# Optimization experiments

Hardware: AMD Instinct MI355X
Metric: run time of the kernel (lower is better)

The kernel has to match this reference:

```python
import jax, jax.numpy as jnp
import numpy as np

B, N, NIN, NHID, D = 8, 2048, 256, 256, 64  # head = 1 (required by squeeze())


def setup_inputs() -> dict:
    key = jax.random.key(0)
    ks = jax.random.split(key, 12)
    xn = lambda k, shape, s=1.0: jax.random.normal(k, shape, jnp.float32) * s
    xav = lambda fi, fo: (2.0 / (fi + fo)) ** 0.5  # xavier_normal std
    return {
        "inputs": xn(ks[0], (B, N, NIN)),
        "fc1_w": xn(ks[1], (NHID, NIN), xav(NIN, NHID)),
        "fc1_b": jnp.full((NHID,), 0.1, jnp.float32),
        "fc2_w": xn(ks[2], (NHID, NHID), xav(NHID, NHID)),
        "fc2_b": jnp.full((NHID,), 0.1, jnp.float32),
        "bn_g": 1.0 + 0.1 * xn(ks[3], (NHID,)),
        "bn_b": 0.1 * xn(ks[4], (NHID,)),
        "bn_mean": 0.1 * xn(ks[5], (NHID,)),
        "bn_var": jax.random.uniform(ks[6], (NHID,), jnp.float32, 0.5, 1.5),
        "wq_w": xn(ks[7], (D, NHID), xav(NHID, D)),
        "wq_b": jnp.full((D,), 0.1, jnp.float32),
        "wk_w": xn(ks[8], (D, NHID), xav(NHID, D)),
        "wk_b": jnp.full((D,), 0.1, jnp.float32),
        "mlp2_w": xn(ks[9], (1, 2 * D), xav(2 * D, 1)),
        "mlp2_b": jnp.full((1,), 0.1, jnp.float32),
    }


def reference(inputs, fc1_w, fc1_b, fc2_w, fc2_b, bn_g, bn_b, bn_mean, bn_var,
              wq_w, wq_b, wk_w, wk_b, mlp2_w, mlp2_b):
    # MLP: Linear -> ELU -> (dropout off, eval) -> Linear -> ELU -> BatchNorm1d (eval, running stats)
    x = jax.nn.elu(jnp.einsum('bni,hi->bnh', inputs, fc1_w) + fc1_b)
    x = jax.nn.elu(jnp.einsum('bnh,oh->bno', x, fc2_w) + fc2_b)
    X = (x - bn_mean) * jax.lax.rsqrt(bn_var + 1e-5) * bn_g + bn_b  # [B,N,NHID]
    # Q/K projections (head=1 -> shapes [B,N,D])
    Xq = jnp.einsum('bnh,dh->bnd', X, wq_w) + wq_b
    Xk = jnp.einsum('bnh,dh->bnd', X, wk_w) + wk_b
    # Original: cat([NK, NQ], -1) over all (i,j) pairs then Linear(2D -> 1).
    # Algebraically identical decomposition: probs[b,i,j] = Xk[b,j].wk_half + Xq[b,i].wq_half + bias
    wk_half, wq_half = mlp2_w[0, :D], mlp2_w[0, D:]
    sk = Xk @ wk_half  # [B,N]  (varies with j, the K/column index)
    sq = Xq @ wq_half  # [B,N]  (varies with i, the Q/row index)
    probs = sq[:, :, None] + sk[:, None, :] + mlp2_b[0]  # [B,N,N]
    return probs
```

## Files before the change

### kernel.cpp

```cpp
#include <hip/hip_runtime.h>
#include <hip/hip_bf16.h>
#include <math.h>

typedef __bf16 bf16x8 __attribute__((ext_vector_type(8)));
typedef float  f32x4  __attribute__((ext_vector_type(4)));
typedef unsigned int u32;
typedef u32 u32x4 __attribute__((ext_vector_type(4)));
typedef unsigned short u16;

#define WS_STG1  0
#define WS_STG2  32768
#define WS_UQ    65536
#define WS_UK    65792
#define WS_CONST 66048
#define WS_SQ    66064
#define WS_SK    82448

__device__ __forceinline__ float elu1(float x) {
    return x > 0.f ? x : (__expf(x) - 1.f);
}

__global__ void prep_all(const float* __restrict__ w1, const float* __restrict__ w2,
                         const float* __restrict__ bn_g, const float* __restrict__ bn_b,
                         const float* __restrict__ bn_mean, const float* __restrict__ bn_var,
                         const float* __restrict__ wq_w, const float* __restrict__ wq_b,
                         const float* __restrict__ wk_w, const float* __restrict__ wk_b,
                         const float* __restrict__ mlp2_w, const float* __restrict__ mlp2_b,
                         float* __restrict__ ws) {
    if (blockIdx.x == 0) {
        __shared__ float redq[256], redk[256];
        const int h = threadIdx.x;
        float s  = bn_g[h] * rsqrtf(bn_var[h] + 1e-5f);
        float tt = bn_b[h] - bn_mean[h] * s;
        float vq = 0.f, vk = 0.f;
        #pragma unroll
        for (int d = 0; d < 64; ++d) {
            vq += wq_w[d * 256 + h] * mlp2_w[64 + d];
            vk += wk_w[d * 256 + h] * mlp2_w[d];
        }
        ws[WS_UQ + h] = s * vq;
        ws[WS_UK + h] = s * vk;
        redq[h] = tt * vq;
        redk[h] = tt * vk;
        __syncthreads();
        for (int st = 128; st > 0; st >>= 1) {
            if (h < st) { redq[h] += redq[h + st]; redk[h] += redk[h + st]; }
            __syncthreads();
        }
        if (h == 0) {
            float cq = 0.f, ck = 0.f;
            for (int d = 0; d < 64; ++d) {
                cq += wq_b[d] * mlp2_w[64 + d];
                ck += wk_b[d] * mlp2_w[d];
            }
            ws[WS_CONST + 0] = redq[0] + cq;
            ws[WS_CONST + 1] = redk[0] + ck;
            ws[WS_CONST + 2] = mlp2_b[0];
        }
        return;
    }
    const int bid = blockIdx.x - 1;
    const int m   = bid >> 3;
    const int kt  = bid & 7;
    const float* src = m ? w2 : w1;
    __bf16* stg = (__bf16*)(ws + (m ? WS_STG2 : WS_STG1));
    const int tid = threadIdx.x;
    #pragma unroll
    for (int it = 0; it < 4; ++it) {
        int idx = it * 256 + tid;
        int nt = idx >> 6, l = idx & 63;
        int lr = l & 15, lk = l >> 4;
        const float* sp = src + (nt * 16 + lr) * 256 + kt * 32 + lk * 8;
        bf16x8 hi;
        #pragma unroll
        for (int j = 0; j < 8; ++j) hi[j] = (__bf16)sp[j];
        *(bf16x8*)(stg + (kt * 16 + nt) * 512 + l * 8) = hi;
    }
}

__global__ __launch_bounds__(512, 4) void main_mfma(const float* __restrict__ inp,
                                                    const float* __restrict__ b1,
                                                    const float* __restrict__ b2,
                                                    float* __restrict__ ws) {
    __shared__ u32 X1p[8192];
    __shared__ float redq[128], redk[128];

    const int tid = threadIdx.x;
    const int l   = tid & 63;
    const int gw  = tid >> 6;
    const int w   = gw & 3;
    const int p   = gw >> 2;
    const int lr  = l & 15;
    const int lk  = l >> 4;
    const int rows0 = blockIdx.x * 32;
    const int koff  = blockIdx.x & 7;
    const int n0  = w * 64;

    const __bf16* s1 = (const __bf16*)(ws + WS_STG1);
    const __bf16* s2 = (const __bf16*)(ws + WS_STG2);
    const float*  arow = inp + (size_t)(rows0 + p * 16 + lr) * 256 + lk * 8;

    f32x4 acc[4];

    #pragma unroll
    for (int nt = 0; nt < 4; ++nt) acc[nt] = (f32x4)0.f;

    bf16x8 bc[4];
    float4 f0, f1;
    {
        const int kts = koff;
        #pragma unroll
        for (int nt = 0; nt < 4; ++nt)
            bc[nt] = *(const bf16x8*)(s1 + ((kts * 16 + w * 4 + nt) << 9) + l * 8);
        f0 = ((const float4*)(arow + kts * 32))[0];
        f1 = ((const float4*)(arow + kts * 32))[1];
    }

    #pragma unroll
    for (int kt = 0; kt < 8; ++kt) {
        bf16x8 bn[4];
        float4 g0 = f0, g1 = f1;
        if (kt < 7) {
            const int ktn = (kt + 1 + koff) & 7;
            #pragma unroll
            for (int nt = 0; nt < 4; ++nt)
                bn[nt] = *(const bf16x8*)(s1 + ((ktn * 16 + w * 4 + nt) << 9) + l * 8);
            g0 = ((const float4*)(arow + ktn * 32))[0];
            g1 = ((const float4*)(arow + ktn * 32))[1];
        } else {
            #pragma unroll
            for (int nt = 0; nt < 4; ++nt) bn[nt] = bc[nt];
        }
        bf16x8 ah, al;
        {
            float fv[8] = {f0.x,f0.y,f0.z,f0.w,f1.x,f1.y,f1.z,f1.w};
            #pragma unroll
            for (int j = 0; j < 8; ++j) {
                __bf16 hv = (__bf16)fv[j];
                ah[j] = hv;
                al[j] = (__bf16)(fv[j] - (float)hv);
            }
        }
        #pragma unroll
        for (int nt = 0; nt < 4; ++nt) {
            acc[nt] = __builtin_amdgcn_mfma_f32_16x16x32_bf16(ah, bc[nt], acc[nt], 0, 0, 0);
            acc[nt] = __builtin_amdgcn_mfma_f32_16x16x32_bf16(al, bc[nt], acc[nt], 0, 0, 0);
        }
        #pragma unroll
        for (int nt = 0; nt < 4; ++nt) bc[nt] = bn[nt];
        f0 = g0; f1 = g1;
    }
    #pragma unroll
    for (int nt = 0; nt < 4; ++nt) {
        int col = n0 + nt * 16 + lr;
        float bb = b1[col];
        #pragma unroll
        for (int r = 0; r < 4; ++r) {
            int row = p * 16 + lk * 4 + r;
            float v = elu1(acc[nt][r] + bb);
            __bf16 hv = (__bf16)v;
            __bf16 lv = (__bf16)(v - (float)hv);
            u32 pk = ((u32)__builtin_bit_cast(u16, hv) << 16) | __builtin_bit_cast(u16, lv);
            int ob = row * 1024 + ((col * 4) ^ ((row & 15) << 4));
            *(u32*)((char*)X1p + ob) = pk;
        }
    }
    __syncthreads();

    #pragma unroll
    for (int nt = 0; nt < 4; ++nt) acc[nt] = (f32x4)0.f;

    const int base = (p * 16 + lr) * 1024;
    const int sw   = lr << 4;

    bf16x8 bc2[4];
    #pragma unroll
    for (int nt = 0; nt < 4; ++nt)
        bc2[nt] = *(const bf16x8*)(s2 + ((koff * 16 + w * 4 + nt) << 9) + l * 8);

    #pragma unroll
    for (int kt = 0; kt < 8; ++kt) {
        const int kts = (kt + koff) & 7;
        bf16x8 bn[4];
        if (kt < 7) {
            const int ktn = (kt + 1 + koff) & 7;
            #pragma unroll
            for (int nt = 0; nt < 4; ++nt)
                bn[nt] = *(const bf16x8*)(s2 + ((ktn * 16 + w * 4 + nt) << 9) + l * 8);
        } else {
            #pragma unroll
            for (int nt = 0; nt < 4; ++nt) bn[nt] = bc2[nt];
        }
        int cb = kts * 128 + lk * 32;
        u32x4 q0 = *(const u32x4*)((const char*)X1p + base + (cb ^ sw));
        u32x4 q1 = *(const u32x4*)((const char*)X1p + base + ((cb + 16) ^ sw));
        u32 hw0 = __builtin_amdgcn_perm(q0.y, q0.x, 0x07060302u);
        u32 hw1 = __builtin_amdgcn_perm(q0.w, q0.z, 0x07060302u);
        u32 hw2 = __builtin_amdgcn_perm(q1.y, q1.x, 0x07060302u);
        u32 hw3 = __builtin_amdgcn_perm(q1.w, q1.z, 0x07060302u);
        u32 lw0 = __builtin_amdgcn_perm(q0.y, q0.x, 0x05040100u);
        u32 lw1 = __builtin_amdgcn_perm(q0.w, q0.z, 0x05040100u);
        u32 lw2 = __builtin_amdgcn_perm(q1.y, q1.x, 0x05040100u);
        u32 lw3 = __builtin_amdgcn_perm(q1.w, q1.z, 0x05040100u);
        u32x4 hh = {hw0, hw1, hw2, hw3};
        u32x4 ll = {lw0, lw1, lw2, lw3};
        bf16x8 ah = __builtin_bit_cast(bf16x8, hh);
        bf16x8 al = __builtin_bit_cast(bf16x8, ll);
        #pragma unroll
        for (int nt = 0; nt < 4; ++nt) {
            acc[nt] = __builtin_amdgcn_mfma_f32_16x16x32_bf16(ah, bc2[nt], acc[nt], 0, 0, 0);
            acc[nt] = __builtin_amdgcn_mfma_f32_16x16x32_bf16(al, bc2[nt], acc[nt], 0, 0, 0);
        }
        #pragma unroll
        for (int nt = 0; nt < 4; ++nt) bc2[nt] = bn[nt];
    }

    float sqp[4] = {0.f,0.f,0.f,0.f};
    float skp[4] = {0.f,0.f,0.f,0.f};
    const float* uq = ws + WS_UQ;
    const float* uk = ws + WS_UK;
    #pragma unroll
    for (int nt = 0; nt < 4; ++nt) {
        int col = n0 + nt * 16 + lr;
        float bb = b2[col], qc = uq[col], kc = uk[col];
        #pragma unroll
        for (int r = 0; r < 4; ++r) {
            float v = elu1(acc[nt][r] + bb);
            sqp[r] += v * qc;
            skp[r] += v * kc;
        }
    }
    #pragma unroll
    for (int mm = 8; mm >= 1; mm >>= 1) {
        #pragma unroll
        for (int r = 0; r < 4; ++r) {
            sqp[r] += __shfl_xor(sqp[r], mm);
            skp[r] += __shfl_xor(skp[r], mm);
        }
    }
    if (lr == 0) {
        #pragma unroll
        for (int r = 0; r < 4; ++r) {
            int rl = lk * 4 + r;
            redq[gw * 16 + rl] = sqp[r];
            redk[gw * 16 + rl] = skp[r];
        }
    }
    __syncthreads();
    if (tid < 32) {
        int pp = tid >> 4, rl = tid & 15;
        float s = ws[WS_CONST + 0];
        #pragma unroll
        for (int ww = 0; ww < 4; ++ww) s += redq[(pp * 4 + ww) * 16 + rl];
        ws[WS_SQ + rows0 + tid] = s;
    } else if (tid < 64) {
        int rr = tid - 32;
        int pp = rr >> 4, rl = rr & 15;
        float s = ws[WS_CONST + 1];
        #pragma unroll
        for (int ww = 0; ww < 4; ++ww) s += redk[(pp * 4 + ww) * 16 + rl];
        ws[WS_SK + rows0 + rr] = s;
    }
}

__global__ __launch_bounds__(256) void broadcast_out(const float* __restrict__ ws,
                                                     float* __restrict__ out) {
    __shared__ float skL[2048];
    const int bi = blockIdx.x;
    const int b = bi >> 8;
    const int chunk = bi & 255;
    const int tid = threadIdx.x;

    float4* skL4 = (float4*)skL;
    const float4* skb4 = (const float4*)(ws + WS_SK + b * 2048);
    #pragma unroll
    for (int it = 0; it < 2; ++it) skL4[it * 256 + tid] = skb4[it * 256 + tid];
    __syncthreads();

    const float mb = ws[WS_CONST + 2];
    const int i0 = chunk * 8;
    #pragma unroll
    for (int i = 0; i < 8; ++i) {
        float sval = ws[WS_SQ + b * 2048 + i0 + i] + mb;
        float4* orow = (float4*)(out + ((size_t)(b * 2048 + i0 + i)) * 2048);
        #pragma unroll
        for (int hh = 0; hh < 2; ++hh) {
            int j4 = hh * 256 + tid;
            float4 v = skL4[j4];
            orow[j4] = make_float4(sval + v.x, sval + v.y, sval + v.z, sval + v.w);
        }
    }
}

extern "C" void kernel_launch(void* const* d_in, const int* in_sizes, int n_in,
                              void* d_out, int out_size, void* d_ws, size_t ws_size,
                              hipStream_t stream) {
    const float* inputs  = (const float*)d_in[0];
    const float* fc1_w   = (const float*)d_in[1];
    const float* fc1_b   = (const float*)d_in[2];
    const float* fc2_w   = (const float*)d_in[3];
    const float* fc2_b   = (const float*)d_in[4];
    const float* bn_g    = (const float*)d_in[5];
    const float* bn_b    = (const float*)d_in[6];
    const float* bn_mean = (const float*)d_in[7];
    const float* bn_var  = (const float*)d_in[8];
    const float* wq_w    = (const float*)d_in[9];
    const float* wq_b    = (const float*)d_in[10];
    const float* wk_w    = (const float*)d_in[11];
    const float* wk_b    = (const float*)d_in[12];
    const float* mlp2_w  = (const float*)d_in[13];
    const float* mlp2_b  = (const float*)d_in[14];
    float* ws  = (float*)d_ws;
    float* out = (float*)d_out;

    hipLaunchKernelGGL(prep_all, dim3(17), dim3(256), 0, stream,
                       fc1_w, fc2_w, bn_g, bn_b, bn_mean, bn_var,
                       wq_w, wq_b, wk_w, wk_b, mlp2_w, mlp2_b, ws);
    hipLaunchKernelGGL(main_mfma, dim3(512), dim3(512), 0, stream,
                       inputs, fc1_b, fc2_b, ws);
    hipLaunchKernelGGL(broadcast_out, dim3(2048), dim3(256), 0, stream, ws, out);
}
```

Baseline: 51.88 us.

## Stage bf16 weight tiles into LDS via global_load_lds instead of per-wave global loads

Both GEMM stages now copy each 32KB chunk of the pre-staged bf16 weights into a shared-memory buffer using direct global-to-LDS loads. Each wave then reads its B fragments from LDS. Before, every wave read the fragments straight from global memory with register prefetching and a per-block k-offset rotation. The goal is to share weight traffic across the block's waves and cut redundant global/L2 reads. In exchange it adds 32KB of LDS, which may lower occupancy, and two barriers per chunk with no double buffering, so load latency is exposed rather than overlapped.

```diff
diff --git a/kernel.cpp b/kernel.cpp
--- a/kernel.cpp
+++ b/kernel.cpp
@@ -18,6 +18,12 @@
 
 __device__ __forceinline__ float elu1(float x) {
     return x > 0.f ? x : (__expf(x) - 1.f);
+}
+
+__device__ __forceinline__ void gload16(const void* g, void* l) {
+    __builtin_amdgcn_global_load_lds((const __attribute__((address_space(1))) void*)g,
+                                     (__attribute__((address_space(3))) void*)l,
+                                     16, 0, 0);
 }
 
 __global__ void prep_all(const float* __restrict__ w1, const float* __restrict__ w2,
@@ -82,6 +88,7 @@
                                                     const float* __restrict__ b1,
                                                     const float* __restrict__ b2,
                                                     float* __restrict__ ws) {
+    __shared__ u32 Wst[8192];
     __shared__ u32 X1p[8192];
     __shared__ float redq[128], redk[128];
 
@@ -93,63 +100,64 @@
     const int lr  = l & 15;
     const int lk  = l >> 4;
     const int rows0 = blockIdx.x * 32;
-    const int koff  = blockIdx.x & 7;
     const int n0  = w * 64;
 
-    const __bf16* s1 = (const __bf16*)(ws + WS_STG1);
-    const __bf16* s2 = (const __bf16*)(ws + WS_STG2);
-    const float*  arow = inp + (size_t)(rows0 + p * 16 + lr) * 256 + lk * 8;
+    const char* stg1b = (const char*)(ws + WS_STG1);
+    const char* stg2b = (const char*)(ws + WS_STG2);
+    const float* arow = inp + (size_t)(rows0 + p * 16 + lr) * 256 + lk * 8;
 
     f32x4 acc[4];
 
     #pragma unroll
     for (int nt = 0; nt < 4; ++nt) acc[nt] = (f32x4)0.f;
 
-    bf16x8 bc[4];
-    float4 f0, f1;
-    {
-        const int kts = koff;
-        #pragma unroll
-        for (int nt = 0; nt < 4; ++nt)
-            bc[nt] = *(const bf16x8*)(s1 + ((kts * 16 + w * 4 + nt) << 9) + l * 8);
-        f0 = ((const float4*)(arow + kts * 32))[0];
-        f1 = ((const float4*)(arow + kts * 32))[1];
-    }
-
-    #pragma unroll
-    for (int kt = 0; kt < 8; ++kt) {
-        bf16x8 bn[4];
-        float4 g0 = f0, g1 = f1;
-        if (kt < 7) {
-            const int ktn = (kt + 1 + koff) & 7;
+    float4 ac0 = ((const float4*)(arow))[0];
+    float4 ac1 = ((const float4*)(arow))[1];
+    float4 ac2 = ((const float4*)(arow + 32))[0];
+    float4 ac3 = ((const float4*)(arow + 32))[1];
+
+    #pragma unroll
+    for (int q = 0; q < 4; ++q) {
+        {
+            const char* src = stg1b + q * 32768;
             #pragma unroll
-            for (int nt = 0; nt < 4; ++nt)
-                bn[nt] = *(const bf16x8*)(s1 + ((ktn * 16 + w * 4 + nt) << 9) + l * 8);
-            g0 = ((const float4*)(arow + ktn * 32))[0];
-            g1 = ((const float4*)(arow + ktn * 32))[1];
-        } else {
+            for (int s = 0; s < 4; ++s)
+                gload16(src + s * 8192 + tid * 16, ((char*)Wst) + s * 8192 + tid * 16);
+        }
+        float4 an0, an1, an2, an3;
+        if (q < 3) {
+            const float* ar = arow + (q + 1) * 64;
+            an0 = ((const float4*)(ar))[0];
+            an1 = ((const float4*)(ar))[1];
+            an2 = ((const float4*)(ar + 32))[0];
+            an3 = ((const float4*)(ar + 32))[1];
+        }
+        __syncthreads();
+        #pragma unroll
+        for (int ktL = 0; ktL < 2; ++ktL) {
+            float4 f0 = ktL ? ac2 : ac0;
+            float4 f1 = ktL ? ac3 : ac1;
+            bf16x8 ah, al;
+            {
+                float fv[8] = {f0.x,f0.y,f0.z,f0.w,f1.x,f1.y,f1.z,f1.w};
+                #pragma unroll
+                for (int j = 0; j < 8; ++j) {
+                    __bf16 hv = (__bf16)fv[j];
+                    ah[j] = hv;
+                    al[j] = (__bf16)(fv[j] - (float)hv);
+                }
+            }
             #pragma unroll
-            for (int nt = 0; nt < 4; ++nt) bn[nt] = bc[nt];
-        }
-        bf16x8 ah, al;
-        {
-            float fv[8] = {f0.x,f0.y,f0.z,f0.w,f1.x,f1.y,f1.z,f1.w};
-            #pragma unroll
-            for (int j = 0; j < 8; ++j) {
-                __bf16 hv = (__bf16)fv[j];
-                ah[j] = hv;
-                al[j] = (__bf16)(fv[j] - (float)hv);
+            for (int nt = 0; nt < 4; ++nt) {
+                bf16x8 b = *(const bf16x8*)((const char*)Wst + (ktL * 16 + w * 4 + nt) * 1024 + l * 16);
+                acc[nt] = __builtin_amdgcn_mfma_f32_16x16x32_bf16(ah, b, acc[nt], 0, 0, 0);
+                acc[nt] = __builtin_amdgcn_mfma_f32_16x16x32_bf16(al, b, acc[nt], 0, 0, 0);
             }
         }
-        #pragma unroll
-        for (int nt = 0; nt < 4; ++nt) {
-            acc[nt] = __builtin_amdgcn_mfma_f32_16x16x32_bf16(ah, bc[nt], acc[nt], 0, 0, 0);
-            acc[nt] = __builtin_amdgcn_mfma_f32_16x16x32_bf16(al, bc[nt], acc[nt], 0, 0, 0);
-        }
-        #pragma unroll
-        for (int nt = 0; nt < 4; ++nt) bc[nt] = bn[nt];
-        f0 = g0; f1 = g1;
-    }
+        __syncthreads();
+        if (q < 3) { ac0 = an0; ac1 = an1; ac2 = an2; ac3 = an3; }
+    }
+
     #pragma unroll
     for (int nt = 0; nt < 4; ++nt) {
         int col = n0 + nt * 16 + lr;
@@ -165,7 +173,6 @@
             *(u32*)((char*)X1p + ob) = pk;
         }
     }
-    __syncthreads();
 
     #pragma unroll
     for (int nt = 0; nt < 4; ++nt) acc[nt] = (f32x4)0.f;
@@ -173,46 +180,41 @@
     const int base = (p * 16 + lr) * 1024;
     const int sw   = lr << 4;
 
-    bf16x8 bc2[4];
-    #pragma unroll
-    for (int nt = 0; nt < 4; ++nt)
-        bc2[nt] = *(const bf16x8*)(s2 + ((koff * 16 + w * 4 + nt) << 9) + l * 8);
-
-    #pragma unroll
-    for (int kt = 0; kt < 8; ++kt) {
-        const int kts = (kt + koff) & 7;
-        bf16x8 bn[4];
-        if (kt < 7) {
-            const int ktn = (kt + 1 + koff) & 7;
+    #pragma unroll
+    for (int q = 0; q < 4; ++q) {
+        {
+            const char* src = stg2b + q * 32768;
             #pragma unroll
-            for (int nt = 0; nt < 4; ++nt)
-                bn[nt] = *(const bf16x8*)(s2 + ((ktn * 16 + w * 4 + nt) << 9) + l * 8);
-        } else {
+            for (int s = 0; s < 4; ++s)
+                gload16(src + s * 8192 + tid * 16, ((char*)Wst) + s * 8192 + tid * 16);
+        }
+        __syncthreads();
+        #pragma unroll
+        for (int ktL = 0; ktL < 2; ++ktL) {
+            const int kt = q * 2 + ktL;
+            int cb = kt * 128 + lk * 32;
+            u32x4 q0 = *(const u32x4*)((const char*)X1p + base + (cb ^ sw));
+            u32x4 q1 = *(const u32x4*)((const char*)X1p + base + ((cb + 16) ^ sw));
+            u32 hw0 = __builtin_amdgcn_perm(q0.y, q0.x, 0x07060302u);
+            u32 hw1 = __builtin_amdgcn_perm(q0.w, q0.z, 0x07060302u);
+            u32 hw2 = __builtin_amdgcn_perm(q1.y, q1.x, 0x07060302u);
+            u32 hw3 = __builtin_amdgcn_perm(q1.w, q1.z, 0x07060302u);
+            u32 lw0 = __builtin_amdgcn_perm(q0.y, q0.x, 0x05040100u);
+            u32 lw1 = __builtin_amdgcn_perm(q0.w, q0.z, 0x05040100u);
+            u32 lw2 = __builtin_amdgcn_perm(q1.y, q1.x, 0x05040100u);
+            u32 lw3 = __builtin_amdgcn_perm(q1.w, q1.z, 0x05040100u);
+            u32x4 hh = {hw0, hw1, hw2, hw3};
+            u32x4 ll = {lw0, lw1, lw2, lw3};
+            bf16x8 ah = __builtin_bit_cast(bf16x8, hh);
+            bf16x8 al = __builtin_bit_cast(bf16x8, ll);
             #pragma unroll
-            for (int nt = 0; nt < 4; ++nt) bn[nt] = bc2[nt];
-        }
-        int cb = kts * 128 + lk * 32;
-        u32x4 q0 = *(const u32x4*)((const char*)X1p + base + (cb ^ sw));
-        u32x4 q1 = *(const u32x4*)((const char*)X1p + base + ((cb + 16) ^ sw));
-        u32 hw0 = __builtin_amdgcn_perm(q0.y, q0.x, 0x07060302u);
-        u32 hw1 = __builtin_amdgcn_perm(q0.w, q0.z, 0x07060302u);
-        u32 hw2 = __builtin_amdgcn_perm(q1.y, q1.x, 0x07060302u);
-        u32 hw3 = __builtin_amdgcn_perm(q1.w, q1.z, 0x07060302u);
-        u32 lw0 = __builtin_amdgcn_perm(q0.y, q0.x, 0x05040100u);
-        u32 lw1 = __builtin_amdgcn_perm(q0.w, q0.z, 0x05040100u);
-        u32 lw2 = __builtin_amdgcn_perm(q1.y, q1.x, 0x05040100u);
-        u32 lw3 = __builtin_amdgcn_perm(q1.w, q1.z, 0x05040100u);
-        u32x4 hh = {hw0, hw1, hw2, hw3};
-        u32x4 ll = {lw0, lw1, lw2, lw3};
-        bf16x8 ah = __builtin_bit_cast(bf16x8, hh);
-        bf16x8 al = __builtin_bit_cast(bf16x8, ll);
-        #pragma unroll
-        for (int nt = 0; nt < 4; ++nt) {
-            acc[nt] = __builtin_amdgcn_mfma_f32_16x16x32_bf16(ah, bc2[nt], acc[nt], 0, 0, 0);
-            acc[nt] = __builtin_amdgcn_mfma_f32_16x16x32_bf16(al, bc2[nt], acc[nt], 0, 0, 0);
-        }
-        #pragma unroll
-        for (int nt = 0; nt < 4; ++nt) bc2[nt] = bn[nt];
+            for (int nt = 0; nt < 4; ++nt) {
+                bf16x8 b = *(const bf16x8*)((const char*)Wst + (ktL * 16 + w * 4 + nt) * 1024 + l * 16);
+                acc[nt] = __builtin_amdgcn_mfma_f32_16x16x32_bf16(ah, b, acc[nt], 0, 0, 0);
+                acc[nt] = __builtin_amdgcn_mfma_f32_16x16x32_bf16(al, b, acc[nt], 0, 0, 0);
+            }
+        }
+        __syncthreads();
     }
 
     float sqp[4] = {0.f,0.f,0.f,0.f};
```

Result: no change. 52.42 us (+1.1%).
